# Kernel optimization log

Hardware: AMD Instinct MI355X
Metric: run time of the kernel (lower is better)

Reference implementation:

```python
import jax, jax.numpy as jnp
import numpy as np


def setup_inputs() -> dict:
    key = jax.random.key(0)
    k1, k2, k3 = jax.random.split(key, 3)
    B, S, I, H, M = 8, 2048, 256, 256, 1024
    x = jax.random.normal(k1, (B, S, I), dtype=jnp.float32)
    mem = jax.random.normal(k2, (B, M, H), dtype=jnp.float32)
    # Xavier-uniform with gain=sqrt(2): bound = sqrt(2)*sqrt(6/(H+I))
    bound = np.sqrt(2.0) * np.sqrt(6.0 / (H + I))
    W = jax.random.uniform(k3, (H, I), dtype=jnp.float32, minval=-bound, maxval=bound)
    return {"x": x, "mem": mem, "W": W}


def reference(x, mem, W):
    # key[b,s,h] = relu(sum_i x[b,s,i] * W[h,i])  -- one batched GEMM for all t
    key_seq = jax.nn.relu(jnp.einsum("bsi,hi->bsh", x, W))
    # val[b,s,m] = sum_h key[b,s,h] * mem[b,m,h]
    val_seq = jnp.einsum("bsh,bmh->bsm", key_seq, mem)
    return key_seq, val_seq
```

## Files before the change

kernel.cpp:

```cpp
#include <hip/hip_runtime.h>
#include <cstdint>

typedef unsigned short u16;
typedef __bf16 bf16x8 __attribute__((ext_vector_type(8)));
typedef float f32x4 __attribute__((ext_vector_type(4)));
typedef u16 u16x8 __attribute__((ext_vector_type(8)));

#define NX   4194304L
#define NMEM 2097152L

__device__ __forceinline__ u16 f2bf(float f) {
  union { float f; uint32_t u; } v; v.f = f;
  uint32_t r = v.u + 0x7fffu + ((v.u >> 16) & 1u);
  return (u16)(r >> 16);
}

__device__ __forceinline__ u16x8 cvt8(float4 a, float4 b) {
  u16x8 o;
  o[0]=f2bf(a.x); o[1]=f2bf(a.y); o[2]=f2bf(a.z); o[3]=f2bf(a.w);
  o[4]=f2bf(b.x); o[5]=f2bf(b.y); o[6]=f2bf(b.z); o[7]=f2bf(b.w);
  return o;
}

__global__ __launch_bounds__(256, 2)
void gemm1_kernel(const float* __restrict__ x, const float* __restrict__ W,
                  float* __restrict__ key_f, u16* __restrict__ key_bf,
                  const float* __restrict__ mem, u16* __restrict__ mem_bf)
{
  constexpr int K = 256;
  __shared__ __align__(16) float sA[128 * 32];
  __shared__ __align__(16) float sB[128 * 32];

  const int tid  = threadIdx.x;
  const int wave = tid >> 6;
  const int lane = tid & 63;
  const int quad = lane >> 4;
  const int r    = lane & 15;
  const int wm   = wave >> 1;
  const int wn   = wave & 1;
  const int bm   = blockIdx.y * 128;
  const int bn   = blockIdx.x * 128;

  const int o_base = wave * 1024 + lane * 16;

  f32x4 acc[4][4];
  #pragma unroll
  for (int i = 0; i < 4; i++)
    #pragma unroll
    for (int j = 0; j < 4; j++)
      acc[i][j] = f32x4{0.f, 0.f, 0.f, 0.f};

  for (int kt = 0; kt < K; kt += 32) {
    __syncthreads();
    #pragma unroll
    for (int rr = 0; rr < 4; rr++) {
      const int o   = rr * 4096 + o_base;
      const int row = o >> 7;
      const int cp  = (o >> 4) & 7;
      const int c   = cp ^ (row & 7);
      const char* ga = (const char*)x + (long)(bm + row) * 1024 + kt * 4 + c * 16;
      const char* gb = (const char*)W + (long)(bn + row) * 1024 + kt * 4 + c * 16;
      char* la = (char*)sA + rr * 4096 + wave * 1024;
      char* lb = (char*)sB + rr * 4096 + wave * 1024;
      __builtin_amdgcn_global_load_lds((const __attribute__((address_space(1))) void*)ga,
                                       (__attribute__((address_space(3))) void*)la, 16, 0, 0);
      __builtin_amdgcn_global_load_lds((const __attribute__((address_space(1))) void*)gb,
                                       (__attribute__((address_space(3))) void*)lb, 16, 0, 0);
    }
    __syncthreads();

    bf16x8 af[4], bfr[4];
    const int s = r & 7;
    #pragma unroll
    for (int i = 0; i < 4; ++i) {
      const float* base = sA + (wm * 64 + i * 16 + r) * 32;
      float4 f0 = *(const float4*)(base + (((2 * quad)     ^ s) << 2));
      float4 f1 = *(const float4*)(base + (((2 * quad + 1) ^ s) << 2));
      u16x8 t = cvt8(f0, f1);
      af[i] = *(bf16x8*)&t;
    }
    #pragma unroll
    for (int j = 0; j < 4; ++j) {
      const float* base = sB + (wn * 64 + j * 16 + r) * 32;
      float4 f0 = *(const float4*)(base + (((2 * quad)     ^ s) << 2));
      float4 f1 = *(const float4*)(base + (((2 * quad + 1) ^ s) << 2));
      u16x8 t = cvt8(f0, f1);
      bfr[j] = *(bf16x8*)&t;
    }
    #pragma unroll
    for (int i = 0; i < 4; ++i)
      #pragma unroll
      for (int j = 0; j < 4; ++j)
        acc[i][j] = __builtin_amdgcn_mfma_f32_16x16x32_bf16(af[i], bfr[j], acc[i][j], 0, 0, 0);
  }

  #pragma unroll
  for (int i = 0; i < 4; i++) {
    #pragma unroll
    for (int j = 0; j < 4; j++) {
      #pragma unroll
      for (int reg = 0; reg < 4; reg++) {
        const int row = bm + wm * 64 + i * 16 + quad * 4 + reg;
        const int col = bn + wn * 64 + j * 16 + r;
        float v = acc[i][j][reg];
        v = v > 0.f ? v : 0.f;
        const long idx = (long)row * 256 + col;
        key_f[idx]  = v;
        key_bf[idx] = f2bf(v);
      }
    }
  }

  {
    const int bid = blockIdx.y * 2 + blockIdx.x;
    const long e0 = ((long)bid * 256 + tid) * 32;
    #pragma unroll
    for (int c = 0; c < 4; ++c) {
      float4 f0 = *(const float4*)(mem + e0 + c * 8);
      float4 f1 = *(const float4*)(mem + e0 + c * 8 + 4);
      *(u16x8*)(mem_bf + e0 + c * 8) = cvt8(f0, f1);
    }
  }
}

__global__ __launch_bounds__(256, 2)
void gemm2_kernel(const u16* __restrict__ A, const u16* __restrict__ B,
                  float* __restrict__ C)
{
  constexpr int K = 256;
  __shared__ __align__(16) u16 sA[128 * 32];
  __shared__ __align__(16) u16 sB[128 * 32];
  const int tid  = threadIdx.x;
  const int wave = tid >> 6;
  const int lane = tid & 63;
  const int quad = lane >> 4;
  const int r    = lane & 15;
  const int wm   = wave >> 1;
  const int wn   = wave & 1;
  const int bm   = blockIdx.y * 128;
  const int bn   = blockIdx.x * 128;
  const int batch = blockIdx.z;

  const char* Ab = (const char*)(A + (long)batch * 2048 * 256);
  const char* Bb = (const char*)(B + (long)batch * 1024 * 256);
  const long ldr = 512;

  f32x4 acc[4][4];
  #pragma unroll
  for (int i = 0; i < 4; i++)
    #pragma unroll
    for (int j = 0; j < 4; j++)
      acc[i][j] = f32x4{0.f, 0.f, 0.f, 0.f};

  const int o0 = wave * 1024 + lane * 16;

  for (int kt = 0; kt < K; kt += 32) {
    __syncthreads();
    #pragma unroll
    for (int rr = 0; rr < 2; rr++) {
      const int o    = rr * 4096 + o0;
      const int row  = o >> 6;
      const int colb = o & 63;
      const char* ga = Ab + (long)(bm + row) * ldr + (long)kt * 2 + colb;
      const char* gb = Bb + (long)(bn + row) * ldr + (long)kt * 2 + colb;
      char* la = (char*)sA + rr * 4096 + wave * 1024;
      char* lb = (char*)sB + rr * 4096 + wave * 1024;
      __builtin_amdgcn_global_load_lds((const __attribute__((address_space(1))) void*)ga,
                                       (__attribute__((address_space(3))) void*)la, 16, 0, 0);
      __builtin_amdgcn_global_load_lds((const __attribute__((address_space(1))) void*)gb,
                                       (__attribute__((address_space(3))) void*)lb, 16, 0, 0);
    }
    __syncthreads();

    bf16x8 af[4], bf[4];
    #pragma unroll
    for (int i = 0; i < 4; i++)
      af[i] = *(const bf16x8*)(sA + (wm * 64 + i * 16 + r) * 32 + quad * 8);
    #pragma unroll
    for (int j = 0; j < 4; j++)
      bf[j] = *(const bf16x8*)(sB + (wn * 64 + j * 16 + r) * 32 + quad * 8);
    #pragma unroll
    for (int i = 0; i < 4; i++)
      #pragma unroll
      for (int j = 0; j < 4; j++)
        acc[i][j] = __builtin_amdgcn_mfma_f32_16x16x32_bf16(af[i], bf[j], acc[i][j], 0, 0, 0);
  }

  float* Co = C + (long)batch * 2048 * 1024;
  #pragma unroll
  for (int i = 0; i < 4; i++) {
    #pragma unroll
    for (int j = 0; j < 4; j++) {
      #pragma unroll
      for (int reg = 0; reg < 4; reg++) {
        const int row = bm + wm * 64 + i * 16 + quad * 4 + reg;
        const int col = bn + wn * 64 + j * 16 + r;
        Co[(long)row * 1024 + col] = acc[i][j][reg];
      }
    }
  }
}

extern "C" void kernel_launch(void* const* d_in, const int* in_sizes, int n_in,
                              void* d_out, int out_size, void* d_ws, size_t ws_size,
                              hipStream_t stream) {
  const float* x   = (const float*)d_in[0];
  const float* mem = (const float*)d_in[1];
  const float* W   = (const float*)d_in[2];
  float* out   = (float*)d_out;
  float* key_f = out;
  float* val_f = out + NX;
  u16* key_bf  = (u16*)d_ws;
  u16* mem_bf  = (u16*)d_ws + NX;

  dim3 g1(2, 128, 1);
  gemm1_kernel<<<g1, 256, 0, stream>>>(x, W, key_f, key_bf, mem, mem_bf);

  dim3 g2(8, 16, 8);
  gemm2_kernel<<<g2, 256, 0, stream>>>(key_bf, mem_bf, val_f);
}
```

Baseline: 129.2 us.

## Drop bf16 workspace copies; gemm2 reads fp32 key and mem directly

Removes the bf16 intermediate buffers for key and mem. gemm1 now stages the whole W tile once into LDS as swizzled bf16 and streams x straight from global memory into registers without per-k syncs. gemm2 loads fp32 key and mem via LDS and converts to bf16 at fragment load. This drops the extra workspace writes and reads, but gemm2 now moves twice the bytes per operand and repeats the conversion across many tiles.

Result: slower. 141.5 us (+9.5%).

```diff
diff --git a/kernel.cpp b/kernel.cpp
--- a/kernel.cpp
+++ b/kernel.cpp
@@ -6,8 +6,7 @@
 typedef float f32x4 __attribute__((ext_vector_type(4)));
 typedef u16 u16x8 __attribute__((ext_vector_type(8)));
 
-#define NX   4194304L
-#define NMEM 2097152L
+#define NX 4194304L
 
 __device__ __forceinline__ u16 f2bf(float f) {
   union { float f; uint32_t u; } v; v.f = f;
@@ -22,14 +21,16 @@
   return o;
 }
 
+__device__ __forceinline__ int sw_addr(int row, int k) {
+  return row * 256 + ((((k >> 3) ^ (row & 7)) << 3)) + (k & 7);
+}
+
 __global__ __launch_bounds__(256, 2)
 void gemm1_kernel(const float* __restrict__ x, const float* __restrict__ W,
-                  float* __restrict__ key_f, u16* __restrict__ key_bf,
-                  const float* __restrict__ mem, u16* __restrict__ mem_bf)
+                  float* __restrict__ key_f)
 {
   constexpr int K = 256;
-  __shared__ __align__(16) float sA[128 * 32];
-  __shared__ __align__(16) float sB[128 * 32];
+  __shared__ __align__(16) u16 sB[128 * 256];
 
   const int tid  = threadIdx.x;
   const int wave = tid >> 6;
@@ -41,7 +42,25 @@
   const int bm   = blockIdx.y * 128;
   const int bn   = blockIdx.x * 128;
 
-  const int o_base = wave * 1024 + lane * 16;
+  {
+    const int rowS = tid >> 1;
+    const int colS = (tid & 1) * 16;
+    const float* Bg = W + (long)(bn + rowS) * K + colS;
+    #pragma unroll
+    for (int c = 0; c < 8; ++c) {
+      const float* p = Bg + c * 32;
+      float4 f0 = *(const float4*)(p);
+      float4 f1 = *(const float4*)(p + 4);
+      float4 f2 = *(const float4*)(p + 8);
+      float4 f3 = *(const float4*)(p + 12);
+      const int col = colS + c * 32;
+      *(u16x8*)(sB + sw_addr(rowS, col))     = cvt8(f0, f1);
+      *(u16x8*)(sB + sw_addr(rowS, col + 8)) = cvt8(f2, f3);
+    }
+  }
+  __syncthreads();
+
+  const float* Af = x + (long)(bm + wm * 64 + r) * K;
 
   f32x4 acc[4][4];
   #pragma unroll
@@ -50,86 +69,48 @@
     for (int j = 0; j < 4; j++)
       acc[i][j] = f32x4{0.f, 0.f, 0.f, 0.f};
 
+  #pragma unroll 2
   for (int kt = 0; kt < K; kt += 32) {
-    __syncthreads();
-    #pragma unroll
-    for (int rr = 0; rr < 4; rr++) {
-      const int o   = rr * 4096 + o_base;
-      const int row = o >> 7;
-      const int cp  = (o >> 4) & 7;
-      const int c   = cp ^ (row & 7);
-      const char* ga = (const char*)x + (long)(bm + row) * 1024 + kt * 4 + c * 16;
-      const char* gb = (const char*)W + (long)(bn + row) * 1024 + kt * 4 + c * 16;
-      char* la = (char*)sA + rr * 4096 + wave * 1024;
-      char* lb = (char*)sB + rr * 4096 + wave * 1024;
-      __builtin_amdgcn_global_load_lds((const __attribute__((address_space(1))) void*)ga,
-                                       (__attribute__((address_space(3))) void*)la, 16, 0, 0);
-      __builtin_amdgcn_global_load_lds((const __attribute__((address_space(1))) void*)gb,
-                                       (__attribute__((address_space(3))) void*)lb, 16, 0, 0);
-    }
-    __syncthreads();
-
-    bf16x8 af[4], bfr[4];
-    const int s = r & 7;
+    bf16x8 af[4], bf[4];
     #pragma unroll
     for (int i = 0; i < 4; ++i) {
-      const float* base = sA + (wm * 64 + i * 16 + r) * 32;
-      float4 f0 = *(const float4*)(base + (((2 * quad)     ^ s) << 2));
-      float4 f1 = *(const float4*)(base + (((2 * quad + 1) ^ s) << 2));
-      u16x8 t = cvt8(f0, f1);
+      const float* p = Af + (long)i * 16 * K + kt + quad * 8;
+      float4 a0 = *(const float4*)(p);
+      float4 a1 = *(const float4*)(p + 4);
+      u16x8 t = cvt8(a0, a1);
       af[i] = *(bf16x8*)&t;
     }
     #pragma unroll
-    for (int j = 0; j < 4; ++j) {
-      const float* base = sB + (wn * 64 + j * 16 + r) * 32;
-      float4 f0 = *(const float4*)(base + (((2 * quad)     ^ s) << 2));
-      float4 f1 = *(const float4*)(base + (((2 * quad + 1) ^ s) << 2));
-      u16x8 t = cvt8(f0, f1);
-      bfr[j] = *(bf16x8*)&t;
-    }
+    for (int j = 0; j < 4; ++j)
+      bf[j] = *(const bf16x8*)(sB + sw_addr(wn * 64 + j * 16 + r, kt + quad * 8));
     #pragma unroll
     for (int i = 0; i < 4; ++i)
       #pragma unroll
       for (int j = 0; j < 4; ++j)
-        acc[i][j] = __builtin_amdgcn_mfma_f32_16x16x32_bf16(af[i], bfr[j], acc[i][j], 0, 0, 0);
+        acc[i][j] = __builtin_amdgcn_mfma_f32_16x16x32_bf16(af[i], bf[j], acc[i][j], 0, 0, 0);
   }
 
   #pragma unroll
-  for (int i = 0; i < 4; i++) {
-    #pragma unroll
-    for (int j = 0; j < 4; j++) {
+  for (int i = 0; i < 4; i++)
+    #pragma unroll
+    for (int j = 0; j < 4; j++)
       #pragma unroll
       for (int reg = 0; reg < 4; reg++) {
         const int row = bm + wm * 64 + i * 16 + quad * 4 + reg;
         const int col = bn + wn * 64 + j * 16 + r;
         float v = acc[i][j][reg];
-        v = v > 0.f ? v : 0.f;
-        const long idx = (long)row * 256 + col;
-        key_f[idx]  = v;
-        key_bf[idx] = f2bf(v);
+        key_f[(long)row * 256 + col] = v > 0.f ? v : 0.f;
       }
-    }
-  }
-
-  {
-    const int bid = blockIdx.y * 2 + blockIdx.x;
-    const long e0 = ((long)bid * 256 + tid) * 32;
-    #pragma unroll
-    for (int c = 0; c < 4; ++c) {
-      float4 f0 = *(const float4*)(mem + e0 + c * 8);
-      float4 f1 = *(const float4*)(mem + e0 + c * 8 + 4);
-      *(u16x8*)(mem_bf + e0 + c * 8) = cvt8(f0, f1);
-    }
-  }
 }
 
 __global__ __launch_bounds__(256, 2)
-void gemm2_kernel(const u16* __restrict__ A, const u16* __restrict__ B,
-                  float* __restrict__ C)
+void gemm2_kernel(const float* __restrict__ key_f, const float* __restrict__ mem,
+                  float* __restrict__ val_f)
 {
   constexpr int K = 256;
-  __shared__ __align__(16) u16 sA[128 * 32];
-  __shared__ __align__(16) u16 sB[128 * 32];
+  __shared__ __align__(16) float sA[128 * 32];
+  __shared__ __align__(16) float sB[128 * 32];
+
   const int tid  = threadIdx.x;
   const int wave = tid >> 6;
   const int lane = tid & 63;
@@ -141,9 +122,10 @@
   const int bn   = blockIdx.x * 128;
   const int batch = blockIdx.z;
 
-  const char* Ab = (const char*)(A + (long)batch * 2048 * 256);
-  const char* Bb = (const char*)(B + (long)batch * 1024 * 256);
-  const long ldr = 512;
+  const char* Ab = (const char*)(key_f + (long)batch * 2048 * 256);
+  const char* Bb = (const char*)(mem   + (long)batch * 1024 * 256);
+
+  const int o_base = wave * 1024 + lane * 16;
 
   f32x4 acc[4][4];
   #pragma unroll
@@ -151,18 +133,17 @@
     #pragma unroll
     for (int j = 0; j < 4; j++)
       acc[i][j] = f32x4{0.f, 0.f, 0.f, 0.f};
-
-  const int o0 = wave * 1024 + lane * 16;
 
   for (int kt = 0; kt < K; kt += 32) {
     __syncthreads();
     #pragma unroll
-    for (int rr = 0; rr < 2; rr++) {
-      const int o    = rr * 4096 + o0;
-      const int row  = o >> 6;
-      const int colb = o & 63;
-      const char* ga = Ab + (long)(bm + row) * ldr + (long)kt * 2 + colb;
-      const char* gb = Bb + (long)(bn + row) * ldr + (long)kt * 2 + colb;
+    for (int rr = 0; rr < 4; rr++) {
+      const int o   = rr * 4096 + o_base;
+      const int row = o >> 7;
+      const int cp  = (o >> 4) & 7;
+      const int c   = cp ^ (row & 7);
+      const char* ga = Ab + (long)(bm + row) * 1024 + kt * 4 + c * 16;
+      const char* gb = Bb + (long)(bn + row) * 1024 + kt * 4 + c * 16;
       char* la = (char*)sA + rr * 4096 + wave * 1024;
       char* lb = (char*)sB + rr * 4096 + wave * 1024;
       __builtin_amdgcn_global_load_lds((const __attribute__((address_space(1))) void*)ga,
@@ -172,33 +153,42 @@
     }
     __syncthreads();
 
-    bf16x8 af[4], bf[4];
-    #pragma unroll
-    for (int i = 0; i < 4; i++)
-      af[i] = *(const bf16x8*)(sA + (wm * 64 + i * 16 + r) * 32 + quad * 8);
-    #pragma unroll
-    for (int j = 0; j < 4; j++)
-      bf[j] = *(const bf16x8*)(sB + (wn * 64 + j * 16 + r) * 32 + quad * 8);
-    #pragma unroll
-    for (int i = 0; i < 4; i++)
-      #pragma unroll
-      for (int j = 0; j < 4; j++)
-        acc[i][j] = __builtin_amdgcn_mfma_f32_16x16x32_bf16(af[i], bf[j], acc[i][j], 0, 0, 0);
+    bf16x8 af[4], bfr[4];
+    const int s = r & 7;
+    #pragma unroll
+    for (int i = 0; i < 4; ++i) {
+      const float* base = sA + (wm * 64 + i * 16 + r) * 32;
+      float4 f0 = *(const float4*)(base + (((2 * quad)     ^ s) << 2));
+      float4 f1 = *(const float4*)(base + (((2 * quad + 1) ^ s) << 2));
+      u16x8 t = cvt8(f0, f1);
+      af[i] = *(bf16x8*)&t;
+    }
+    #pragma unroll
+    for (int j = 0; j < 4; ++j) {
+      const float* base = sB + (wn * 64 + j * 16 + r) * 32;
+      float4 f0 = *(const float4*)(base + (((2 * quad)     ^ s) << 2));
+      float4 f1 = *(const float4*)(base + (((2 * quad + 1) ^ s) << 2));
+      u16x8 t = cvt8(f0, f1);
+      bfr[j] = *(bf16x8*)&t;
+    }
+    #pragma unroll
+    for (int i = 0; i < 4; ++i)
+      #pragma unroll
+      for (int j = 0; j < 4; ++j)
+        acc[i][j] = __builtin_amdgcn_mfma_f32_16x16x32_bf16(af[i], bfr[j], acc[i][j], 0, 0, 0);
   }
 
-  float* Co = C + (long)batch * 2048 * 1024;
-  #pragma unroll
-  for (int i = 0; i < 4; i++) {
-    #pragma unroll
-    for (int j = 0; j < 4; j++) {
+  float* Co = val_f + (long)batch * 2048 * 1024;
+  #pragma unroll
+  for (int i = 0; i < 4; i++)
+    #pragma unroll
+    for (int j = 0; j < 4; j++)
       #pragma unroll
       for (int reg = 0; reg < 4; reg++) {
         const int row = bm + wm * 64 + i * 16 + quad * 4 + reg;
         const int col = bn + wn * 64 + j * 16 + r;
         Co[(long)row * 1024 + col] = acc[i][j][reg];
       }
-    }
-  }
 }
 
 extern "C" void kernel_launch(void* const* d_in, const int* in_sizes, int n_in,
@@ -210,12 +200,11 @@
   float* out   = (float*)d_out;
   float* key_f = out;
   float* val_f = out + NX;
-  u16* key_bf  = (u16*)d_ws;
-  u16* mem_bf  = (u16*)d_ws + NX;
+  (void)d_ws; (void)ws_size;
 
   dim3 g1(2, 128, 1);
-  gemm1_kernel<<<g1, 256, 0, stream>>>(x, W, key_f, key_bf, mem, mem_bf);
+  gemm1_kernel<<<g1, 256, 0, stream>>>(x, W, key_f);
 
   dim3 g2(8, 16, 8);
-  gemm2_kernel<<<g2, 256, 0, stream>>>(key_bf, mem_bf, val_f);
-}
+  gemm2_kernel<<<g2, 256, 0, stream>>>(key_f, mem, val_f);
+}
```
